# Performance work log

Hardware: AMD Instinct MI355X
Metric: run time of the kernel (lower is better)

## Reference

```python
import jax, jax.numpy as jnp
import numpy as np

B, N, D = 4, 4096, 256

def setup_inputs() -> dict:
    key = jax.random.key(0)
    ks = jax.random.split(key, 7)
    def xavier(k, shape):
        fan_in, fan_out = shape[1], shape[0]
        a = jnp.sqrt(6.0 / (fan_in + fan_out))
        return jax.random.uniform(k, shape, jnp.float32, -a, a)
    return {
        "x": jax.random.normal(ks[0], (B, N, D), jnp.float32),
        "Wq": xavier(ks[1], (D, D)),
        "bq": jnp.zeros((D,), jnp.float32),
        "Wk": xavier(ks[2], (D, D)),
        "bk": jnp.zeros((D,), jnp.float32),
        "Wv": xavier(ks[3], (D, D)),
        "bv": jnp.zeros((D,), jnp.float32),
        "scale": jnp.asarray([jnp.sqrt(jnp.float32(D))]),
    }

def reference(x, Wq, bq, Wk, bk, Wv, bv, scale):
    # nn.Linear: y = x @ W.T + b
    q = jnp.einsum('bnd,ed->bne', x, Wq) + bq
    k = jnp.einsum('bnd,ed->bne', x, Wk) + bk
    v = jnp.einsum('bnd,ed->bne', x, Wv) + bv
    scores = jnp.einsum('bqd,bkd->bqk', q, k) / scale[0]  # [B,N,N]
    attn = jax.nn.softmax(scores, axis=-1)
    out = jnp.einsum('bqk,bkd->bqd', attn, v)
    return out
```

## Files before the change

### kernel.cpp

```cpp
#include <hip/hip_runtime.h>
#include <hip/hip_bf16.h>

typedef unsigned int u32;
typedef unsigned short u16;
typedef __attribute__((ext_vector_type(8))) __bf16 bf8v;
typedef __attribute__((ext_vector_type(16))) float f32x16;
typedef __attribute__((ext_vector_type(8))) u16 u16x8;

__device__ inline u16 f2bf(float f) {
    u32 u = __float_as_uint(f);
    u = (u + 0x7FFF + ((u >> 16) & 1)) >> 16;
    return (u16)u;
}
__device__ inline u32 pk2(float a, float b) {
    return (u32)f2bf(a) | ((u32)f2bf(b) << 16);
}
__device__ inline float bf2f(u16 h) { return __uint_as_float(((u32)h) << 16); }

__device__ inline void dma16(const u16* g, u16* l) {
    __builtin_amdgcn_global_load_lds(
        (const __attribute__((address_space(1))) void*)g,
        (__attribute__((address_space(3))) void*)l, 16, 0, 0);
}

__global__ void cvt_all(const float* __restrict__ x,
                        const float* __restrict__ wq, const float* __restrict__ wk,
                        const float* __restrict__ wv,
                        u16* __restrict__ xp, u16* __restrict__ wall) {
    const int blk = blockIdx.x;
    if (blk < 2048) {
        int g = blk * 256 + threadIdx.x;
        int row = g >> 5, cp = g & 31;
        const float* s = x + row * 256 + cp * 8;
        float4 a = *(const float4*)s;
        float4 b = *(const float4*)(s + 4);
        uint4 o;
        o.x = pk2(a.x, a.y); o.y = pk2(a.z, a.w);
        o.z = pk2(b.x, b.y); o.w = pk2(b.z, b.w);
        *(uint4*)(xp + (row >> 5) * 8192 + cp * 256 + (row & 31) * 8) = o;
    } else {
        const int bb = blk - 2048;
        const int m = bb >> 5;
        const float* src = m == 0 ? wq : m == 1 ? wk : wv;
        int g = (bb & 31) * 256 + threadIdx.x;
        int row = g >> 5, c = g & 31;
        const float* s = src + row * 256 + c * 8;
        float4 a = *(const float4*)s;
        float4 b = *(const float4*)(s + 4);
        uint4 o;
        o.x = pk2(a.x, a.y); o.y = pk2(a.z, a.w);
        o.z = pk2(b.x, b.y); o.w = pk2(b.z, b.w);
        *(uint4*)(wall + m * 65536 + row * 256 + ((c ^ (row & 7)) * 8)) = o;
    }
}

__global__ __launch_bounds__(256) void qkv_proj(
    const u16* __restrict__ xp, const u16* __restrict__ wall,
    const float* __restrict__ bq, const float* __restrict__ bk, const float* __restrict__ bv,
    u16* __restrict__ qp, u16* __restrict__ kp, u16* __restrict__ vp)
{
    __shared__ u16 Ws[64 * 256];

    const int blk = blockIdx.x;
    const int xcd = blk & 7;
    const int s2 = blk >> 3;
    const int rt = s2 / 12;
    const int yz = s2 % 12;
    const int sel = yz >> 2;
    const int colbase = (yz & 3) * 64;
    const int rowbase0 = (xcd * 16 + rt) * 128;

    const float* bias = sel == 0 ? bq : sel == 1 ? bk : bv;
    const int tid = threadIdx.x;
    const int wave = tid >> 6, lane = tid & 63;
    const int l31 = lane & 31, l5 = lane >> 5;
    const int tg = (rowbase0 >> 5) + wave;

    {
        const u16* wsrc = wall + sel * 65536 + colbase * 256;
#pragma unroll
        for (int j = 0; j < 8; j++) {
            const int i = wave * 8 + j;
            dma16(wsrc + i * 512 + lane * 8, Ws + i * 512);
        }
    }
    asm volatile("s_waitcnt vmcnt(0)" ::: "memory");
    __syncthreads();

    f32x16 acc0, acc1;
#pragma unroll
    for (int j = 0; j < 16; j++) { acc0[j] = 0.f; acc1[j] = 0.f; }

    const u16* ap = xp + tg * 8192 + l5 * 256 + l31 * 8;
    const int sw = l31 & 7;
#pragma unroll
    for (int kk = 0; kk < 16; kk++) {
        bf8v af = *(const bf8v*)(ap + kk * 512);
        bf8v b0 = *(const bf8v*)(Ws + l31 * 256 + (((kk * 2 + l5) ^ sw) * 8));
        bf8v b1 = *(const bf8v*)(Ws + (32 + l31) * 256 + (((kk * 2 + l5) ^ sw) * 8));
        acc0 = __builtin_amdgcn_mfma_f32_32x32x16_bf16(af, b0, acc0, 0, 0, 0);
        acc1 = __builtin_amdgcn_mfma_f32_32x32x16_bf16(af, b1, acc1, 0, 0, 0);
    }

    const float bias0 = bias[colbase + l31], bias1 = bias[colbase + 32 + l31];
    if (sel < 2) {
        u16* base = (sel == 0 ? qp : kp) + tg * 8192;
        const int c0 = (colbase >> 3) + (l31 >> 3), j0 = l31 & 7;
#pragma unroll
        for (int r = 0; r < 16; r++) {
            const int R = (r & 3) + 8 * (r >> 2) + 4 * l5;
            base[c0 * 256 + R * 8 + j0]       = f2bf(acc0[r] + bias0);
            base[(c0 + 4) * 256 + R * 8 + j0] = f2bf(acc1[r] + bias1);
        }
    } else {
        u16* base = vp + tg * 8192;
        const int d0 = colbase + l31, d1 = d0 + 32;
#pragma unroll
        for (int r = 0; r < 16; r++) {
            const int R = (r & 3) + 8 * (r >> 2) + 4 * l5;
            base[(R >> 3) * 2048 + d0 * 8 + (R & 7)] = f2bf(acc0[r] + bias0);
            base[(R >> 3) * 2048 + d1 * 8 + (R & 7)] = f2bf(acc1[r] + bias1);
        }
    }
}

__global__ __launch_bounds__(256, 2) void flash_attn(
    const u16* __restrict__ qp_, const u16* __restrict__ kp_, const u16* __restrict__ vp_,
    const float* __restrict__ scale,
    u16* __restrict__ Opb, float* __restrict__ ml)
{
    __shared__ u16 Ks[2 * 8192];
    __shared__ u16 Vs[2 * 8192];
    __shared__ u16 Ps[4 * 1152];

    const int tid = threadIdx.x;
    const int wave = tid >> 6, lane = tid & 63;
    const int l31 = lane & 31, l5 = lane >> 5;

    const int blk = blockIdx.x;
    const int slot = blk >> 3;
    const int g = (blk & 7) * 2 + (slot >> 5);
    const int qtile = slot & 31;
    const int b = g >> 2, s = g & 3;
    const int qbase = qtile * 128 + wave * 32;
    const float inv_scale = 1.0f / scale[0];

    union { u16x8 u; bf8v v; } oneu;
#pragma unroll
    for (int j = 0; j < 8; j++) oneu.u[j] = 0x3F80;
    const bf8v ones = oneu.v;

    bf8v qf[16];
    {
        const u16* qp = qp_ + (b * 128 + qtile * 4 + wave) * 8192 + l31 * 8;
#pragma unroll
        for (int kk = 0; kk < 16; kk++)
            qf[kk] = *(const bf8v*)(qp + (kk * 2 + l5) * 256);
    }

    f32x16 o[8];
#pragma unroll
    for (int i = 0; i < 8; i++)
#pragma unroll
        for (int j = 0; j < 16; j++) o[i][j] = 0.f;
    f32x16 ls;
#pragma unroll
    for (int j = 0; j < 16; j++) ls[j] = 0.f;

    const u16* kbase = kp_ + (b * 128 + s * 32) * 8192;
    const u16* vbase = vp_ + (b * 128 + s * 32) * 8192;
    u16* pw = Ps + wave * 1152;

#pragma unroll
    for (int j = 0; j < 4; j++) {
        const int i = wave * 4 + j;
        dma16(kbase + i * 512 + lane * 8, Ks + i * 512);
    }
#pragma unroll
    for (int j = 0; j < 4; j++) {
        const int i = wave * 4 + j;
        dma16(vbase + i * 512 + lane * 8, Vs + i * 512);
    }
#pragma unroll
    for (int j = 0; j < 4; j++) {
        const int i = wave * 4 + j;
        dma16(kbase + 8192 + i * 512 + lane * 8, Ks + 8192 + i * 512);
    }
    asm volatile("s_waitcnt vmcnt(8)" ::: "memory");
    asm volatile("s_barrier" ::: "memory");

    bf8v pf0, pf1;
    {
        f32x16 c;
#pragma unroll
        for (int j = 0; j < 16; j++) c[j] = 0.f;
#pragma unroll
        for (int kk = 0; kk < 16; kk++) {
            bf8v kf = *(const bf8v*)(Ks + (kk * 2 + l5) * 256 + l31 * 8);
            c = __builtin_amdgcn_mfma_f32_32x32x16_bf16(qf[kk], kf, c, 0, 0, 0);
        }
#pragma unroll
        for (int r = 0; r < 16; r++) {
            const int R = (r & 3) + 8 * (r >> 2) + 4 * l5;
            pw[R * 36 + l31] = f2bf(__expf(c[r] * inv_scale));
        }
        asm volatile("s_waitcnt lgkmcnt(0)" ::: "memory");
        pf0 = *(const bf8v*)(pw + l31 * 36 + l5 * 8);
        pf1 = *(const bf8v*)(pw + l31 * 36 + 16 + l5 * 8);
    }

#pragma unroll 1
    for (int it = 0; it < 31; it++) {
        const int buf = it & 1;
        asm volatile("s_waitcnt vmcnt(0)" ::: "memory");
        asm volatile("s_barrier" ::: "memory");
        {
            const u16* vt_ = vbase + (it + 1) * 8192;
#pragma unroll
            for (int j = 0; j < 4; j++) {
                const int i = wave * 4 + j;
                dma16(vt_ + i * 512 + lane * 8, Vs + (buf ^ 1) * 8192 + i * 512);
            }
            if (it < 30) {
                const u16* kt_ = kbase + (it + 2) * 8192;
#pragma unroll
                for (int j = 0; j < 4; j++) {
                    const int i = wave * 4 + j;
                    dma16(kt_ + i * 512 + lane * 8, Ks + buf * 8192 + i * 512);
                }
            }
        }
        const u16* Kb_ = Ks + (buf ^ 1) * 8192;
        f32x16 c;
#pragma unroll
        for (int j = 0; j < 16; j++) c[j] = 0.f;
#pragma unroll
        for (int kk = 0; kk < 16; kk++) {
            bf8v kf = *(const bf8v*)(Kb_ + (kk * 2 + l5) * 256 + l31 * 8);
            c = __builtin_amdgcn_mfma_f32_32x32x16_bf16(qf[kk], kf, c, 0, 0, 0);
        }
        const u16* Vb_ = Vs + buf * 8192;
        ls = __builtin_amdgcn_mfma_f32_32x32x16_bf16(pf0, ones, ls, 0, 0, 0);
        ls = __builtin_amdgcn_mfma_f32_32x32x16_bf16(pf1, ones, ls, 0, 0, 0);
#pragma unroll
        for (int j = 0; j < 8; j++) {
            bf8v vf0 = *(const bf8v*)(Vb_ + (l5 * 256 + j * 32 + l31) * 8);
            o[j] = __builtin_amdgcn_mfma_f32_32x32x16_bf16(pf0, vf0, o[j], 0, 0, 0);
            {
                const int r = 2 * j;
                const int R = (r & 3) + 8 * (r >> 2) + 4 * l5;
                pw[R * 36 + l31] = f2bf(__expf(c[r] * inv_scale));
            }
            bf8v vf1 = *(const bf8v*)(Vb_ + ((2 + l5) * 256 + j * 32 + l31) * 8);
            o[j] = __builtin_amdgcn_mfma_f32_32x32x16_bf16(pf1, vf1, o[j], 0, 0, 0);
            {
                const int r = 2 * j + 1;
                const int R = (r & 3) + 8 * (r >> 2) + 4 * l5;
                pw[R * 36 + l31] = f2bf(__expf(c[r] * inv_scale));
            }
        }
        asm volatile("s_waitcnt lgkmcnt(0)" ::: "memory");
        pf0 = *(const bf8v*)(pw + l31 * 36 + l5 * 8);
        pf1 = *(const bf8v*)(pw + l31 * 36 + 16 + l5 * 8);
    }

    asm volatile("s_waitcnt vmcnt(0)" ::: "memory");
    asm volatile("s_barrier" ::: "memory");
    {
        const u16* Vb_ = Vs + 8192;
        ls = __builtin_amdgcn_mfma_f32_32x32x16_bf16(pf0, ones, ls, 0, 0, 0);
        ls = __builtin_amdgcn_mfma_f32_32x32x16_bf16(pf1, ones, ls, 0, 0, 0);
#pragma unroll
        for (int j = 0; j < 8; j++) {
            bf8v vf0 = *(const bf8v*)(Vb_ + (l5 * 256 + j * 32 + l31) * 8);
            o[j] = __builtin_amdgcn_mfma_f32_32x32x16_bf16(pf0, vf0, o[j], 0, 0, 0);
            bf8v vf1 = *(const bf8v*)(Vb_ + ((2 + l5) * 256 + j * 32 + l31) * 8);
            o[j] = __builtin_amdgcn_mfma_f32_32x32x16_bf16(pf1, vf1, o[j], 0, 0, 0);
        }
    }

    const int rowg = s * 16384 + b * 4096 + qbase;
    u16* ob = Opb + (size_t)rowg * 256;
#pragma unroll
    for (int nb = 0; nb < 8; nb++)
#pragma unroll
        for (int r = 0; r < 16; r++) {
            const int R = (r & 3) + 8 * (r >> 2) + 4 * l5;
            ob[R * 256 + nb * 32 + l31] = f2bf(o[nb][r]);
        }
    if (l31 == 0)
#pragma unroll
        for (int r = 0; r < 16; r++) {
            const int R = (r & 3) + 8 * (r >> 2) + 4 * l5;
            ml[rowg + R] = ls[r];
        }
}

__global__ __launch_bounds__(256) void combine(
    const u16* __restrict__ Opb, const float* __restrict__ ml, float* __restrict__ out)
{
    const int row = blockIdx.x * 4 + (threadIdx.x >> 6);
    const int lane = threadIdx.x & 63;
    const float denom = ml[row] + ml[16384 + row] + ml[32768 + row] + ml[49152 + row];
    float4 acc = {0.f, 0.f, 0.f, 0.f};
#pragma unroll
    for (int si = 0; si < 4; si++) {
        ushort4 v = *(const ushort4*)(Opb + ((size_t)si * 16384 + row) * 256 + lane * 4);
        acc.x += bf2f(v.x); acc.y += bf2f(v.y);
        acc.z += bf2f(v.z); acc.w += bf2f(v.w);
    }
    const float inv = 1.0f / denom;
    acc.x *= inv; acc.y *= inv; acc.z *= inv; acc.w *= inv;
    *((float4*)(out + (size_t)row * 256) + lane) = acc;
}

extern "C" void kernel_launch(void* const* d_in, const int* in_sizes, int n_in,
                              void* d_out, int out_size, void* d_ws, size_t ws_size,
                              hipStream_t stream) {
    const float* x     = (const float*)d_in[0];
    const float* Wq    = (const float*)d_in[1];
    const float* bq    = (const float*)d_in[2];
    const float* Wk    = (const float*)d_in[3];
    const float* bk    = (const float*)d_in[4];
    const float* Wv    = (const float*)d_in[5];
    const float* bv    = (const float*)d_in[6];
    const float* scale = (const float*)d_in[7];
    float* out = (float*)d_out;

    char* ws = (char*)d_ws;
    u16* xp   = (u16*)ws;
    u16* qp   = (u16*)(ws + (8u  << 20));
    u16* kp   = (u16*)(ws + (16u << 20));
    u16* vp   = (u16*)(ws + (24u << 20));
    u16* wall = (u16*)(ws + (32u << 20));
    u16* Opb  = (u16*)(ws + (34u << 20));
    float* ml = (float*)(ws + (66u << 20));

    cvt_all<<<2144, 256, 0, stream>>>(x, Wq, Wk, Wv, xp, wall);
    qkv_proj<<<1536, 256, 0, stream>>>(xp, wall, bq, bk, bv, qp, kp, vp);
    flash_attn<<<512, 256, 0, stream>>>(qp, kp, vp, scale, Opb, ml);
    combine<<<4096, 256, 0, stream>>>(Opb, ml, out);
}
```

Before: 180.0 us.

## Interleave QK^T and PV MFMAs with split accumulators and raised wave priority

Splits the QK^T accumulation into two independent accumulator chains and interleaves those MFMAs with the PV MFMAs inside one loop. The exp/pack of scores moves after the MFMA block. The exponential becomes exp2f with a folded log2e scale, and s_setprio brackets the MFMA region. The goal is to break the serial dependency chain on a single accumulator and keep the matrix pipe busy. In exchange it needs more accumulator registers and takes the exp work off the MFMA shadow, which could hurt occupancy or overlap.

```diff
diff --git a/kernel.cpp b/kernel.cpp
--- a/kernel.cpp
+++ b/kernel.cpp
@@ -143,7 +143,7 @@
     const int qtile = slot & 31;
     const int b = g >> 2, s = g & 3;
     const int qbase = qtile * 128 + wave * 32;
-    const float inv_scale = 1.0f / scale[0];
+    const float is2 = 1.44269504088896f / scale[0];
 
     union { u16x8 u; bf8v v; } oneu;
 #pragma unroll
@@ -191,18 +191,20 @@
 
     bf8v pf0, pf1;
     {
-        f32x16 c;
-#pragma unroll
-        for (int j = 0; j < 16; j++) c[j] = 0.f;
-#pragma unroll
-        for (int kk = 0; kk < 16; kk++) {
-            bf8v kf = *(const bf8v*)(Ks + (kk * 2 + l5) * 256 + l31 * 8);
-            c = __builtin_amdgcn_mfma_f32_32x32x16_bf16(qf[kk], kf, c, 0, 0, 0);
-        }
-#pragma unroll
-        for (int r = 0; r < 16; r++) {
-            const int R = (r & 3) + 8 * (r >> 2) + 4 * l5;
-            pw[R * 36 + l31] = f2bf(__expf(c[r] * inv_scale));
+        f32x16 c0, c1;
+#pragma unroll
+        for (int j = 0; j < 16; j++) { c0[j] = 0.f; c1[j] = 0.f; }
+#pragma unroll
+        for (int j = 0; j < 8; j++) {
+            bf8v kf0 = *(const bf8v*)(Ks + (j * 2 + l5) * 256 + l31 * 8);
+            c0 = __builtin_amdgcn_mfma_f32_32x32x16_bf16(qf[j], kf0, c0, 0, 0, 0);
+            bf8v kf1 = *(const bf8v*)(Ks + ((8 + j) * 2 + l5) * 256 + l31 * 8);
+            c1 = __builtin_amdgcn_mfma_f32_32x32x16_bf16(qf[8 + j], kf1, c1, 0, 0, 0);
+        }
+#pragma unroll
+        for (int r = 0; r < 16; r++) {
+            const int R = (r & 3) + 8 * (r >> 2) + 4 * l5;
+            pw[R * 36 + l31] = f2bf(exp2f((c0[r] + c1[r]) * is2));
         }
         asm volatile("s_waitcnt lgkmcnt(0)" ::: "memory");
         pf0 = *(const bf8v*)(pw + l31 * 36 + l5 * 8);
@@ -214,6 +216,17 @@
         const int buf = it & 1;
         asm volatile("s_waitcnt vmcnt(0)" ::: "memory");
         asm volatile("s_barrier" ::: "memory");
+
+        const u16* Kb_ = Ks + (buf ^ 1) * 8192;
+        const u16* Vb_ = Vs + buf * 8192;
+
+        __builtin_amdgcn_s_setprio(1);
+        f32x16 c0, c1;
+#pragma unroll
+        for (int j = 0; j < 16; j++) { c0[j] = 0.f; c1[j] = 0.f; }
+        ls = __builtin_amdgcn_mfma_f32_32x32x16_bf16(pf0, ones, ls, 0, 0, 0);
+        ls = __builtin_amdgcn_mfma_f32_32x32x16_bf16(pf1, ones, ls, 0, 0, 0);
+
         {
             const u16* vt_ = vbase + (it + 1) * 8192;
 #pragma unroll
@@ -230,34 +243,24 @@
                 }
             }
         }
-        const u16* Kb_ = Ks + (buf ^ 1) * 8192;
-        f32x16 c;
-#pragma unroll
-        for (int j = 0; j < 16; j++) c[j] = 0.f;
-#pragma unroll
-        for (int kk = 0; kk < 16; kk++) {
-            bf8v kf = *(const bf8v*)(Kb_ + (kk * 2 + l5) * 256 + l31 * 8);
-            c = __builtin_amdgcn_mfma_f32_32x32x16_bf16(qf[kk], kf, c, 0, 0, 0);
-        }
-        const u16* Vb_ = Vs + buf * 8192;
-        ls = __builtin_amdgcn_mfma_f32_32x32x16_bf16(pf0, ones, ls, 0, 0, 0);
-        ls = __builtin_amdgcn_mfma_f32_32x32x16_bf16(pf1, ones, ls, 0, 0, 0);
+
 #pragma unroll
         for (int j = 0; j < 8; j++) {
+            bf8v kf0 = *(const bf8v*)(Kb_ + (j * 2 + l5) * 256 + l31 * 8);
+            c0 = __builtin_amdgcn_mfma_f32_32x32x16_bf16(qf[j], kf0, c0, 0, 0, 0);
             bf8v vf0 = *(const bf8v*)(Vb_ + (l5 * 256 + j * 32 + l31) * 8);
             o[j] = __builtin_amdgcn_mfma_f32_32x32x16_bf16(pf0, vf0, o[j], 0, 0, 0);
-            {
-                const int r = 2 * j;
-                const int R = (r & 3) + 8 * (r >> 2) + 4 * l5;
-                pw[R * 36 + l31] = f2bf(__expf(c[r] * inv_scale));
-            }
+            bf8v kf1 = *(const bf8v*)(Kb_ + ((8 + j) * 2 + l5) * 256 + l31 * 8);
+            c1 = __builtin_amdgcn_mfma_f32_32x32x16_bf16(qf[8 + j], kf1, c1, 0, 0, 0);
             bf8v vf1 = *(const bf8v*)(Vb_ + ((2 + l5) * 256 + j * 32 + l31) * 8);
             o[j] = __builtin_amdgcn_mfma_f32_32x32x16_bf16(pf1, vf1, o[j], 0, 0, 0);
-            {
-                const int r = 2 * j + 1;
-                const int R = (r & 3) + 8 * (r >> 2) + 4 * l5;
-                pw[R * 36 + l31] = f2bf(__expf(c[r] * inv_scale));
-            }
+        }
+        __builtin_amdgcn_s_setprio(0);
+
+#pragma unroll
+        for (int r = 0; r < 16; r++) {
+            const int R = (r & 3) + 8 * (r >> 2) + 4 * l5;
+            pw[R * 36 + l31] = f2bf(exp2f((c0[r] + c1[r]) * is2));
         }
         asm volatile("s_waitcnt lgkmcnt(0)" ::: "memory");
         pf0 = *(const bf8v*)(pw + l31 * 36 + l5 * 8);
@@ -268,6 +271,7 @@
     asm volatile("s_barrier" ::: "memory");
     {
         const u16* Vb_ = Vs + 8192;
+        __builtin_amdgcn_s_setprio(1);
         ls = __builtin_amdgcn_mfma_f32_32x32x16_bf16(pf0, ones, ls, 0, 0, 0);
         ls = __builtin_amdgcn_mfma_f32_32x32x16_bf16(pf1, ones, ls, 0, 0, 0);
 #pragma unroll
@@ -277,6 +281,7 @@
             bf8v vf1 = *(const bf8v*)(Vb_ + ((2 + l5) * 256 + j * 32 + l31) * 8);
             o[j] = __builtin_amdgcn_mfma_f32_32x32x16_bf16(pf1, vf1, o[j], 0, 0, 0);
         }
+        __builtin_amdgcn_s_setprio(0);
     }
 
     const int rowg = s * 16384 + b * 4096 + qbase;
```

After: 202.9 us. 1.13x slower.
